# Kernel tuning notes

Hardware: AMD Instinct MI355X
Metric: run time of the kernel (lower is better)

## Reference

```python
import jax, jax.numpy as jnp
import numpy as np

B, T, D_IN, H, NUM_CLASSES = 512, 1024, 4, 64, 1098


def setup_inputs() -> dict:
    key = jax.random.key(0)
    ks = jax.random.split(key, 20)
    s = 1.0 / np.sqrt(H)  # PyTorch LSTM init range

    def w(k, shape):
        return jax.random.uniform(k, shape, jnp.float32, -s, s)

    inp = {}
    inp['x'] = jax.random.normal(ks[0], (B, T, D_IN), jnp.float32)
    lens = jax.random.randint(ks[1], (B,), 1, T + 1)
    inp['lengths'] = jnp.sort(lens)[::-1]  # descending, like pack_sequence
    i = 2
    for layer, d in ((0, D_IN), (1, 2 * H)):
        for dirn in ('f', 'b'):
            inp[f'W_ih_l{layer}{dirn}'] = w(ks[i], (4 * H, d)); i += 1
            inp[f'W_hh_l{layer}{dirn}'] = w(ks[i], (4 * H, H)); i += 1
            inp[f'b_ih_l{layer}{dirn}'] = w(ks[i], (4 * H,)); i += 1
            inp[f'b_hh_l{layer}{dirn}'] = w(ks[i], (4 * H,)); i += 1
    inp['W_out'] = w(ks[i], (NUM_CLASSES, 2 * H)); i += 1
    inp['b_out'] = w(ks[i], (NUM_CLASSES,))
    return inp


def _lstm_layer(x, W_ih, W_hh, b_ih, b_hh):
    # x: [B, T, D] -> outputs [B, T, H]; PyTorch gate order i, f, g, o
    Bb = x.shape[0]
    Hh = W_hh.shape[1]
    xW = jnp.einsum('btd,gd->btg', x, W_ih) + b_ih + b_hh  # [B, T, 4H]

    def step(carry, xt):
        h, c = carry
        g = xt + h @ W_hh.T
        i, f, gg, o = jnp.split(g, 4, axis=-1)
        c = jax.nn.sigmoid(f) * c + jax.nn.sigmoid(i) * jnp.tanh(gg)
        h = jax.nn.sigmoid(o) * jnp.tanh(c)
        return (h, c), h

    init = (jnp.zeros((Bb, Hh), x.dtype), jnp.zeros((Bb, Hh), x.dtype))
    _, hs = jax.lax.scan(step, init, jnp.swapaxes(xW, 0, 1))
    return jnp.swapaxes(hs, 0, 1)


def _reverse_padded(x, lengths):
    # per-sequence time reversal within the valid length (packed-seq semantics)
    Tt = x.shape[1]
    t = jnp.arange(Tt)
    idx = jnp.where(t[None, :] < lengths[:, None], lengths[:, None] - 1 - t[None, :], t[None, :])
    return jnp.take_along_axis(x, idx[:, :, None], axis=1)


def _bidir_layer(x, lengths, pf, pb):
    hf = _lstm_layer(x, *pf)
    hb = _reverse_padded(_lstm_layer(_reverse_padded(x, lengths), *pb), lengths)
    return jnp.concatenate([hf, hb], axis=-1)


def reference(x, lengths,
              W_ih_l0f, W_hh_l0f, b_ih_l0f, b_hh_l0f,
              W_ih_l0b, W_hh_l0b, b_ih_l0b, b_hh_l0b,
              W_ih_l1f, W_hh_l1f, b_ih_l1f, b_hh_l1f,
              W_ih_l1b, W_hh_l1b, b_ih_l1b, b_hh_l1b,
              W_out, b_out):
    h = _bidir_layer(x, lengths,
                     (W_ih_l0f, W_hh_l0f, b_ih_l0f, b_hh_l0f),
                     (W_ih_l0b, W_hh_l0b, b_ih_l0b, b_hh_l0b))
    h = _bidir_layer(h, lengths,
                     (W_ih_l1f, W_hh_l1f, b_ih_l1f, b_hh_l1f),
                     (W_ih_l1b, W_hh_l1b, b_ih_l1b, b_hh_l1b))
    # gather last valid timestep per sequence: [B, 2H]
    lasts = jnp.take_along_axis(h, (lengths - 1)[:, None, None], axis=1)[:, 0]
    return lasts @ W_out.T + b_out
```

## Files before the change

kernel.cpp:

```cpp
#include <hip/hip_runtime.h>
#include <stdint.h>

#define BATCH 512
#define TMAX  1024
#define NC    1098
#define H     64
#define CH    8

typedef __attribute__((ext_vector_type(2))) float    v2;
typedef __attribute__((ext_vector_type(2))) _Float16 h2;

__device__ __forceinline__ v2 mkv2(float a, float b) { v2 r; r.x = a; r.y = b; return r; }
__device__ __forceinline__ float sigmoidf_(float x) { return 1.0f / (1.0f + __expf(-x)); }
__device__ __forceinline__ float tanhf_(float x) { return 1.0f - 2.0f / (__expf(2.0f * x) + 1.0f); }
__device__ __forceinline__ h2 u2h(uint32_t u) { union { uint32_t u; h2 h; } c; c.u = u; return c.h; }

__device__ __forceinline__ float fdot2_(h2 w, h2 x, float acc) {
    return __builtin_amdgcn_fdot2(w, x, acc, false);
}

__global__ __launch_bounds__(256) void lstm_l0(
    const float* __restrict__ x, const int* __restrict__ lengths,
    const float* __restrict__ Wih_f, const float* __restrict__ Whh_f,
    const float* __restrict__ bih_f, const float* __restrict__ bhh_f,
    const float* __restrict__ Wih_b, const float* __restrict__ Whh_b,
    const float* __restrict__ bih_b, const float* __restrict__ bhh_b,
    _Float16* __restrict__ h0 )
{
    const int bk = blockIdx.x;
    const int t = threadIdx.x;
    const int j = t & 63, w = t >> 6;
    const int seq = (w < 2) ? bk : (BATCH - 1 - bk);
    const int dir = w & 1;
    const int xb  = w >> 1;
    const int L = lengths[seq];

    const float* Wih = dir ? Wih_b : Wih_f;
    const float* Whh = dir ? Whh_b : Whh_f;
    const float* bih = dir ? bih_b : bih_f;
    const float* bhh = dir ? bhh_b : bhh_f;

    h2 wh[4][32];
    #pragma unroll
    for (int g = 0; g < 4; g++) {
        const float4* pw = (const float4*)(Whh + (size_t)(64*g + j) * H);
        #pragma unroll
        for (int k = 0; k < 16; k++) {
            float4 a = pw[k];
            h2 lo; lo.x = (_Float16)a.x; lo.y = (_Float16)a.y;
            h2 hi; hi.x = (_Float16)a.z; hi.y = (_Float16)a.w;
            wh[g][2*k]   = lo;
            wh[g][2*k+1] = hi;
        }
    }
    float4 wx[4]; float bb[4];
    #pragma unroll
    for (int g = 0; g < 4; g++) {
        wx[g] = ((const float4*)Wih)[64*g + j];
        bb[g] = bih[64*g + j] + bhh[64*g + j];
    }

    __shared__ __align__(16) float4    xbuf[2][TMAX];
    __shared__ __align__(16) _Float16  hln[4][H];
    {
        const int sA = bk, sB = BATCH - 1 - bk;
        const int LA = lengths[sA], LB = lengths[sB];
        const float4* xA = (const float4*)x + (size_t)sA * TMAX;
        const float4* xB = (const float4*)x + (size_t)sB * TMAX;
        for (int i = t; i < LA; i += 256) xbuf[0][i] = xA[i];
        for (int i = t; i < LB; i += 256) xbuf[1][i] = xB[i];
    }
    hln[w][j] = (_Float16)0.0f;
    float c = 0.0f;
    __syncthreads();

    _Float16* outp = h0 + (size_t)seq * TMAX * 128 + dir * H + j;

    for (int s = 0; s < L; s++) {
        const int tt = dir ? (L - 1 - s) : s;
        const float4 xt = xbuf[xb][tt];
        float p[4];
        #pragma unroll
        for (int g = 0; g < 4; g++)
            p[g] = fmaf(wx[g].w, xt.w, fmaf(wx[g].z, xt.z,
                   fmaf(wx[g].y, xt.y, fmaf(wx[g].x, xt.x, bb[g]))));
        float acA[4] = {0.f,0.f,0.f,0.f}, acB[4] = {0.f,0.f,0.f,0.f};
        const uint4* h4 = (const uint4*)&hln[w][0];
        #pragma unroll
        for (int q = 0; q < 8; q++) {
            uint4 u = h4[q];
            h2 p0 = u2h(u.x), p1 = u2h(u.y), p2 = u2h(u.z), p3 = u2h(u.w);
            #pragma unroll
            for (int g = 0; g < 4; g++) {
                acA[g] = fdot2_(wh[g][4*q+0], p0, acA[g]);
                acA[g] = fdot2_(wh[g][4*q+1], p1, acA[g]);
                acB[g] = fdot2_(wh[g][4*q+2], p2, acB[g]);
                acB[g] = fdot2_(wh[g][4*q+3], p3, acB[g]);
            }
        }
        #pragma unroll
        for (int g = 0; g < 4; g++) p[g] += acA[g] + acB[g];
        const float gi = sigmoidf_(p[0]);
        const float gf = sigmoidf_(p[1]);
        const float gg = tanhf_(p[2]);
        const float go = sigmoidf_(p[3]);
        c = fmaf(gf, c, gi * gg);
        const float h = go * tanhf_(c);
        hln[w][j] = (_Float16)h;
        outp[(size_t)tt * 128] = (_Float16)h;
    }
}

__global__ __launch_bounds__(384) void lstm_l1(
    const _Float16* __restrict__ h0, const int* __restrict__ lengths,
    const float* __restrict__ Wih,  const float* __restrict__ Whh,
    const float* __restrict__ bih,  const float* __restrict__ bhh,
    const float* __restrict__ WihB, const float* __restrict__ bihB,
    const float* __restrict__ bhhB,
    const float* __restrict__ Wout, const float* __restrict__ bout,
    float* __restrict__ out)
{
    const int bk = blockIdx.x;
    const int t = threadIdx.x;
    const int grp = (t >= 192) ? 1 : 0;
    const int tl = t - 192 * grp;
    const int wl = tl >> 6;
    const int l = tl & 63;
    const int seq = grp ? (BATCH - 1 - bk) : bk;
    const int L = lengths[seq];
    const int nch = (L + CH - 1) / CH;
    const int nchMax = (lengths[bk] + CH - 1) / CH;

    __shared__ __align__(16) float    xw[2][2][CH][256];
    __shared__ __align__(16) _Float16 hst[2][2][CH][128];
    __shared__ __align__(16) _Float16 hln[2][H];
    __shared__ __align__(16) float    ybuf[2][2*H];
    __shared__ __align__(16) float    gb[2][192];
    __shared__ __align__(16) float    h0r[2][128];

    const _Float16* hseq = h0 + (size_t)seq * TMAX * 128;

    h2 wsh[128];
    float bb[4] = {0.f, 0.f, 0.f, 0.f};
    int rA = 0, rB = 0;
    if (wl == 0) {
        #pragma unroll
        for (int g = 0; g < 4; g++) {
            const float4* pw = (const float4*)(Whh + (size_t)(64*g + l) * H);
            #pragma unroll
            for (int k = 0; k < 16; k++) {
                float4 a = pw[k];
                h2 lo; lo.x = (_Float16)a.x; lo.y = (_Float16)a.y;
                h2 hi; hi.x = (_Float16)a.z; hi.y = (_Float16)a.w;
                wsh[g*32 + 2*k]   = lo;
                wsh[g*32 + 2*k+1] = hi;
            }
            bb[g] = bih[64*g + l] + bhh[64*g + l];
        }
        hln[grp][l] = (_Float16)0.0f;
    } else {
        const int pw = wl - 1;
        rA = pw * 128 + l; rB = pw * 128 + 64 + l;
        const float4* pa = (const float4*)(Wih + (size_t)rA * 128);
        const float4* pb = (const float4*)(Wih + (size_t)rB * 128);
        #pragma unroll
        for (int k = 0; k < 32; k++) {
            float4 a = pa[k], b2 = pb[k];
            h2 alo; alo.x = (_Float16)a.x;  alo.y = (_Float16)a.y;
            h2 ahi; ahi.x = (_Float16)a.z;  ahi.y = (_Float16)a.w;
            h2 blo; blo.x = (_Float16)b2.x; blo.y = (_Float16)b2.y;
            h2 bhi; bhi.x = (_Float16)b2.z; bhi.y = (_Float16)b2.w;
            wsh[2*k]        = alo;
            wsh[2*k + 1]    = ahi;
            wsh[64 + 2*k]   = blo;
            wsh[64 + 2*k+1] = bhi;
        }
    }

    uint4 st0;
    auto stage_load = [&](int ck) {
        const uint4* gp = (const uint4*)(hseq + (size_t)ck * CH * 128);
        st0 = gp[(wl - 1) * 64 + l];
    };
    auto stage_store = [&](int ck) {
        uint4* dp = (uint4*)&hst[grp][ck & 1][0][0];
        dp[(wl - 1) * 64 + l] = st0;
    };
    auto produce = [&](int ck) {
        const int par = ck & 1;
        for (int r = 0; r < CH; r++) {
            const uint4* rp = (const uint4*)&hst[grp][par][r][0];
            float aA = 0.f, aB = 0.f;
            #pragma unroll
            for (int q = 0; q < 16; q++) {
                uint4 u = rp[q];
                h2 p0 = u2h(u.x), p1 = u2h(u.y), p2 = u2h(u.z), p3 = u2h(u.w);
                aA = fdot2_(wsh[4*q+0], p0, aA);
                aA = fdot2_(wsh[4*q+1], p1, aA);
                aA = fdot2_(wsh[4*q+2], p2, aA);
                aA = fdot2_(wsh[4*q+3], p3, aA);
                aB = fdot2_(wsh[64+4*q+0], p0, aB);
                aB = fdot2_(wsh[64+4*q+1], p1, aB);
                aB = fdot2_(wsh[64+4*q+2], p2, aB);
                aB = fdot2_(wsh[64+4*q+3], p3, aB);
            }
            xw[grp][par][r][rA] = aA;
            xw[grp][par][r][rB] = aB;
        }
    };

    float c = 0.f, h = 0.f;

    if (wl >= 1) { stage_load(0); stage_store(0); if (nch > 1) stage_load(1); }
    __syncthreads();
    if (wl >= 1) { produce(0); if (nch > 1) stage_store(1); }
    __syncthreads();

    for (int cc = 0; cc < nchMax; cc++) {
        if (wl == 0) {
            const int sbeg = cc * CH;
            const int send = (sbeg + CH < L) ? (sbeg + CH) : L;
            const int par = cc & 1;
            for (int s = sbeg; s < send; s++) {
                const int r = s - sbeg;
                float p[4];
                #pragma unroll
                for (int g = 0; g < 4; g++)
                    p[g] = xw[grp][par][r][g*64 + l] + bb[g];
                float acA[4] = {0.f,0.f,0.f,0.f}, acB[4] = {0.f,0.f,0.f,0.f};
                const uint4* h4 = (const uint4*)&hln[grp][0];
                #pragma unroll
                for (int q = 0; q < 8; q++) {
                    uint4 u = h4[q];
                    h2 p0 = u2h(u.x), p1 = u2h(u.y), p2 = u2h(u.z), p3 = u2h(u.w);
                    #pragma unroll
                    for (int g = 0; g < 4; g++) {
                        acA[g] = fdot2_(wsh[g*32+4*q+0], p0, acA[g]);
                        acA[g] = fdot2_(wsh[g*32+4*q+1], p1, acA[g]);
                        acB[g] = fdot2_(wsh[g*32+4*q+2], p2, acB[g]);
                        acB[g] = fdot2_(wsh[g*32+4*q+3], p3, acB[g]);
                    }
                }
                #pragma unroll
                for (int g = 0; g < 4; g++) p[g] += acA[g] + acB[g];
                const float gi = sigmoidf_(p[0]);
                const float gf = sigmoidf_(p[1]);
                const float gg = tanhf_(p[2]);
                const float go = sigmoidf_(p[3]);
                c = fmaf(gf, c, gi * gg);
                h = go * tanhf_(c);
                hln[grp][l] = (_Float16)h;
            }
        } else {
            if (cc + 2 < nch) stage_load(cc + 2);
            if (cc + 1 < nch) produce(cc + 1);
            if (cc + 2 < nch) stage_store(cc + 2);
        }
        __syncthreads();
    }

    if (wl == 0) ybuf[grp][l] = h;
    if (tl < 128) h0r[grp][tl] = (float)hseq[(size_t)(L - 1) * 128 + tl];
    __syncthreads();
    {
        const int row = (tl < 64) ? tl : (tl + 64);
        const float4* wr = (const float4*)(WihB + (size_t)row * 128);
        const float4* xr = (const float4*)&h0r[grp][0];
        v2 a0 = mkv2(bihB[row] + bhhB[row], 0.f), a1 = mkv2(0.f, 0.f);
        #pragma unroll
        for (int k = 0; k < 32; k++) {
            float4 wv = wr[k], xv = xr[k];
            a0 += mkv2(wv.x, wv.y) * mkv2(xv.x, xv.y);
            a1 += mkv2(wv.z, wv.w) * mkv2(xv.z, xv.w);
        }
        const float a = (a0.x + a0.y) + (a1.x + a1.y);
        gb[grp][tl] = (tl >= 64 && tl < 128) ? tanhf_(a) : sigmoidf_(a);
    }
    __syncthreads();
    if (tl < 64) {
        const float hb = gb[grp][128 + tl] * tanhf_(gb[grp][tl] * gb[grp][64 + tl]);
        ybuf[grp][H + tl] = hb;
    }
    __syncthreads();
    const float4* yv = (const float4*)&ybuf[grp][0];
    for (int o = tl; o < NC; o += 192) {
        const float4* wr = (const float4*)(Wout + (size_t)o * 128);
        v2 a0 = mkv2(bout[o], 0.f), a1 = mkv2(0.f, 0.f);
        #pragma unroll
        for (int k = 0; k < 32; k++) {
            float4 wv = wr[k], yy = yv[k];
            a0 += mkv2(wv.x, wv.y) * mkv2(yy.x, yy.y);
            a1 += mkv2(wv.z, wv.w) * mkv2(yy.z, yy.w);
        }
        out[(size_t)seq * NC + o] = (a0.x + a0.y) + (a1.x + a1.y);
    }
}

extern "C" void kernel_launch(void* const* d_in, const int* in_sizes, int n_in,
                              void* d_out, int out_size, void* d_ws, size_t ws_size,
                              hipStream_t stream) {
    const float* x        = (const float*)d_in[0];
    const int*   lengths  = (const int*)  d_in[1];
    const float* Wih_l0f  = (const float*)d_in[2];
    const float* Whh_l0f  = (const float*)d_in[3];
    const float* bih_l0f  = (const float*)d_in[4];
    const float* bhh_l0f  = (const float*)d_in[5];
    const float* Wih_l0b  = (const float*)d_in[6];
    const float* Whh_l0b  = (const float*)d_in[7];
    const float* bih_l0b  = (const float*)d_in[8];
    const float* bhh_l0b  = (const float*)d_in[9];
    const float* Wih_l1f  = (const float*)d_in[10];
    const float* Whh_l1f  = (const float*)d_in[11];
    const float* bih_l1f  = (const float*)d_in[12];
    const float* bhh_l1f  = (const float*)d_in[13];
    const float* Wih_l1b  = (const float*)d_in[14];
    const float* bih_l1b  = (const float*)d_in[16];
    const float* bhh_l1b  = (const float*)d_in[17];
    const float* Wout     = (const float*)d_in[18];
    const float* bout     = (const float*)d_in[19];
    float* out = (float*)d_out;

    _Float16* h0 = (_Float16*)d_ws;

    lstm_l0<<<dim3(BATCH / 2), 256, 0, stream>>>(
        x, lengths,
        Wih_l0f, Whh_l0f, bih_l0f, bhh_l0f,
        Wih_l0b, Whh_l0b, bih_l0b, bhh_l0b, h0);

    lstm_l1<<<dim3(BATCH / 2), 384, 0, stream>>>(
        h0, lengths,
        Wih_l1f, Whh_l1f, bih_l1f, bhh_l1f,
        Wih_l1b, bih_l1b, bhh_l1b, Wout, bout, out);
}
```

Baseline: 1.212 ms.

## Batch 16 sequences per block and use MFMA for layer-0 LSTM recurrence

Layer 0 is restructured so each block handles 16 sequences in one direction, and the recurrent and input projections run as 16x16x32 f16 MFMAs instead of per-thread fdot2 loops. The h state is double-buffered in shared memory with one block barrier per step, and x is prefetched one step ahead from global memory. The grid shrinks from 256 to 64 blocks, so fewer CUs are used. Each block now iterates for the longest length in its group, which wastes steps on shorter sequences.

Result: slower. 1.849 ms (+52.6%).

```diff
diff --git a/kernel.cpp b/kernel.cpp
--- a/kernel.cpp
+++ b/kernel.cpp
@@ -6,9 +6,12 @@
 #define NC    1098
 #define H     64
 #define CH    8
+#define G16   16
 
 typedef __attribute__((ext_vector_type(2))) float    v2;
 typedef __attribute__((ext_vector_type(2))) _Float16 h2;
+typedef __attribute__((ext_vector_type(8))) _Float16 f16x8;
+typedef __attribute__((ext_vector_type(4))) float    f32x4;
 
 __device__ __forceinline__ v2 mkv2(float a, float b) { v2 r; r.x = a; r.y = b; return r; }
 __device__ __forceinline__ float sigmoidf_(float x) { return 1.0f / (1.0f + __expf(-x)); }
@@ -27,87 +30,121 @@
     const float* __restrict__ bih_b, const float* __restrict__ bhh_b,
     _Float16* __restrict__ h0 )
 {
-    const int bk = blockIdx.x;
-    const int t = threadIdx.x;
-    const int j = t & 63, w = t >> 6;
-    const int seq = (w < 2) ? bk : (BATCH - 1 - bk);
-    const int dir = w & 1;
-    const int xb  = w >> 1;
-    const int L = lengths[seq];
+    const int bid = blockIdx.x;
+    const int dir = bid >> 5;
+    const int g   = bid & 31;
+    const int t   = threadIdx.x;
+    const int w   = t >> 6;
+    const int l   = t & 63;
+    const int q   = l >> 4;
+    const int m16 = l & 15;
 
     const float* Wih = dir ? Wih_b : Wih_f;
     const float* Whh = dir ? Whh_b : Whh_f;
     const float* bih = dir ? bih_b : bih_f;
     const float* bhh = dir ? bhh_b : bhh_f;
 
-    h2 wh[4][32];
+    f16x8 bf[4][2];
+    f16x8 bx[4];
+    float bb[4];
     #pragma unroll
-    for (int g = 0; g < 4; g++) {
-        const float4* pw = (const float4*)(Whh + (size_t)(64*g + j) * H);
-        #pragma unroll
-        for (int k = 0; k < 16; k++) {
-            float4 a = pw[k];
-            h2 lo; lo.x = (_Float16)a.x; lo.y = (_Float16)a.y;
-            h2 hi; hi.x = (_Float16)a.z; hi.y = (_Float16)a.w;
-            wh[g][2*k]   = lo;
-            wh[g][2*k+1] = hi;
-        }
-    }
-    float4 wx[4]; float bb[4];
+    for (int tt = 0; tt < 4; tt++) {
+        const int row = tt*64 + 16*w + m16;
+        #pragma unroll
+        for (int kk = 0; kk < 2; kk++) {
+            const float4* p4 = (const float4*)(Whh + (size_t)row * H + kk*32 + 8*q);
+            float4 v0 = p4[0], v1 = p4[1];
+            f16x8 f;
+            f[0]=(_Float16)v0.x; f[1]=(_Float16)v0.y; f[2]=(_Float16)v0.z; f[3]=(_Float16)v0.w;
+            f[4]=(_Float16)v1.x; f[5]=(_Float16)v1.y; f[6]=(_Float16)v1.z; f[7]=(_Float16)v1.w;
+            bf[tt][kk] = f;
+        }
+        f16x8 fx;
+        #pragma unroll
+        for (int j = 0; j < 8; j++) fx[j] = (_Float16)0.0f;
+        if (q == 0) {
+            const float4 xv = *(const float4*)(Wih + (size_t)row * 4);
+            fx[0]=(_Float16)xv.x; fx[1]=(_Float16)xv.y;
+            fx[2]=(_Float16)xv.z; fx[3]=(_Float16)xv.w;
+        }
+        bx[tt] = fx;
+        bb[tt] = bih[row] + bhh[row];
+    }
+
+    const int nsteps = lengths[G16 * g];
+    const int LrA = lengths[G16*g + m16];
+    int Ls[4];
     #pragma unroll
-    for (int g = 0; g < 4; g++) {
-        wx[g] = ((const float4*)Wih)[64*g + j];
-        bb[g] = bih[64*g + j] + bhh[64*g + j];
-    }
-
-    __shared__ __align__(16) float4    xbuf[2][TMAX];
-    __shared__ __align__(16) _Float16  hln[4][H];
-    {
-        const int sA = bk, sB = BATCH - 1 - bk;
-        const int LA = lengths[sA], LB = lengths[sB];
-        const float4* xA = (const float4*)x + (size_t)sA * TMAX;
-        const float4* xB = (const float4*)x + (size_t)sB * TMAX;
-        for (int i = t; i < LA; i += 256) xbuf[0][i] = xA[i];
-        for (int i = t; i < LB; i += 256) xbuf[1][i] = xB[i];
-    }
-    hln[w][j] = (_Float16)0.0f;
-    float c = 0.0f;
-    __syncthreads();
-
-    _Float16* outp = h0 + (size_t)seq * TMAX * 128 + dir * H + j;
-
-    for (int s = 0; s < L; s++) {
-        const int tt = dir ? (L - 1 - s) : s;
-        const float4 xt = xbuf[xb][tt];
-        float p[4];
-        #pragma unroll
-        for (int g = 0; g < 4; g++)
-            p[g] = fmaf(wx[g].w, xt.w, fmaf(wx[g].z, xt.z,
-                   fmaf(wx[g].y, xt.y, fmaf(wx[g].x, xt.x, bb[g]))));
-        float acA[4] = {0.f,0.f,0.f,0.f}, acB[4] = {0.f,0.f,0.f,0.f};
-        const uint4* h4 = (const uint4*)&hln[w][0];
-        #pragma unroll
-        for (int q = 0; q < 8; q++) {
-            uint4 u = h4[q];
-            h2 p0 = u2h(u.x), p1 = u2h(u.y), p2 = u2h(u.z), p3 = u2h(u.w);
-            #pragma unroll
-            for (int g = 0; g < 4; g++) {
-                acA[g] = fdot2_(wh[g][4*q+0], p0, acA[g]);
-                acA[g] = fdot2_(wh[g][4*q+1], p1, acA[g]);
-                acB[g] = fdot2_(wh[g][4*q+2], p2, acB[g]);
-                acB[g] = fdot2_(wh[g][4*q+3], p3, acB[g]);
+    for (int r = 0; r < 4; r++) Ls[r] = lengths[G16*g + 4*q + r];
+
+    __shared__ _Float16 Hb[2][16][72];
+    for (int i = t; i < 2*16*72; i += 256) (&Hb[0][0][0])[i] = (_Float16)0.0f;
+    __syncthreads();
+
+    float c4[4] = {0.f, 0.f, 0.f, 0.f};
+    const float* xrowA = x + (size_t)(G16*g + m16) * TMAX * 4;
+
+    float4 xcur = make_float4(0.f, 0.f, 0.f, 0.f);
+    if (q == 0) {
+        const int tt0 = dir ? (LrA - 1) : 0;
+        xcur = *(const float4*)(xrowA + (size_t)tt0 * 4);
+    }
+
+    int p = 0;
+    for (int s = 0; s < nsteps; s++) {
+        f16x8 a0 = *(const f16x8*)&Hb[p][m16][8*q];
+        f16x8 a1 = *(const f16x8*)&Hb[p][m16][32 + 8*q];
+        f16x8 ax;
+        #pragma unroll
+        for (int j = 0; j < 8; j++) ax[j] = (_Float16)0.0f;
+        if (q == 0) {
+            ax[0]=(_Float16)xcur.x; ax[1]=(_Float16)xcur.y;
+            ax[2]=(_Float16)xcur.z; ax[3]=(_Float16)xcur.w;
+        }
+        float4 xnxt = make_float4(0.f, 0.f, 0.f, 0.f);
+        if (q == 0 && s + 1 < nsteps) {
+            int tn = dir ? (LrA - 2 - s) : (s + 1);
+            tn = tn < 0 ? 0 : (tn >= LrA ? LrA - 1 : tn);
+            xnxt = *(const float4*)(xrowA + (size_t)tn * 4);
+        }
+
+        f32x4 acc0, acc1, acc2, acc3;
+        acc0[0]=bb[0]; acc0[1]=bb[0]; acc0[2]=bb[0]; acc0[3]=bb[0];
+        acc1[0]=bb[1]; acc1[1]=bb[1]; acc1[2]=bb[1]; acc1[3]=bb[1];
+        acc2[0]=bb[2]; acc2[1]=bb[2]; acc2[2]=bb[2]; acc2[3]=bb[2];
+        acc3[0]=bb[3]; acc3[1]=bb[3]; acc3[2]=bb[3]; acc3[3]=bb[3];
+        acc0 = __builtin_amdgcn_mfma_f32_16x16x32_f16(a0, bf[0][0], acc0, 0,0,0);
+        acc1 = __builtin_amdgcn_mfma_f32_16x16x32_f16(a0, bf[1][0], acc1, 0,0,0);
+        acc2 = __builtin_amdgcn_mfma_f32_16x16x32_f16(a0, bf[2][0], acc2, 0,0,0);
+        acc3 = __builtin_amdgcn_mfma_f32_16x16x32_f16(a0, bf[3][0], acc3, 0,0,0);
+        acc0 = __builtin_amdgcn_mfma_f32_16x16x32_f16(a1, bf[0][1], acc0, 0,0,0);
+        acc1 = __builtin_amdgcn_mfma_f32_16x16x32_f16(a1, bf[1][1], acc1, 0,0,0);
+        acc2 = __builtin_amdgcn_mfma_f32_16x16x32_f16(a1, bf[2][1], acc2, 0,0,0);
+        acc3 = __builtin_amdgcn_mfma_f32_16x16x32_f16(a1, bf[3][1], acc3, 0,0,0);
+        acc0 = __builtin_amdgcn_mfma_f32_16x16x32_f16(ax, bx[0], acc0, 0,0,0);
+        acc1 = __builtin_amdgcn_mfma_f32_16x16x32_f16(ax, bx[1], acc1, 0,0,0);
+        acc2 = __builtin_amdgcn_mfma_f32_16x16x32_f16(ax, bx[2], acc2, 0,0,0);
+        acc3 = __builtin_amdgcn_mfma_f32_16x16x32_f16(ax, bx[3], acc3, 0,0,0);
+
+        #pragma unroll
+        for (int r = 0; r < 4; r++) {
+            const float gi = sigmoidf_(acc0[r]);
+            const float gf = sigmoidf_(acc1[r]);
+            const float gg = tanhf_(acc2[r]);
+            const float go = sigmoidf_(acc3[r]);
+            c4[r] = fmaf(gf, c4[r], gi * gg);
+            const float hv = go * tanhf_(c4[r]);
+            const _Float16 hf = (_Float16)hv;
+            Hb[p ^ 1][4*q + r][16*w + m16] = hf;
+            if (s < Ls[r]) {
+                const int seq = G16*g + 4*q + r;
+                const int trt = dir ? (Ls[r] - 1 - s) : s;
+                h0[((size_t)seq * TMAX + trt) * 128 + dir*64 + 16*w + m16] = hf;
             }
         }
-        #pragma unroll
-        for (int g = 0; g < 4; g++) p[g] += acA[g] + acB[g];
-        const float gi = sigmoidf_(p[0]);
-        const float gf = sigmoidf_(p[1]);
-        const float gg = tanhf_(p[2]);
-        const float go = sigmoidf_(p[3]);
-        c = fmaf(gf, c, gi * gg);
-        const float h = go * tanhf_(c);
-        hln[w][j] = (_Float16)h;
-        outp[(size_t)tt * 128] = (_Float16)h;
+        xcur = xnxt;
+        __syncthreads();
+        p ^= 1;
     }
 }
 
@@ -322,7 +359,7 @@
 
     _Float16* h0 = (_Float16*)d_ws;
 
-    lstm_l0<<<dim3(BATCH / 2), 256, 0, stream>>>(
+    lstm_l0<<<dim3(64), 256, 0, stream>>>(
         x, lengths,
         Wih_l0f, Whh_l0f, bih_l0f, bhh_l0f,
         Wih_l0b, Whh_l0b, bih_l0b, bhh_l0b, h0);
```

## Interleave two sequences per wave in layer-0 LSTM to hide recurrence latency

Applied to the files above, without the earlier changes.

Each wave now processes two independent sequences (a long and a short one paired from each end of the length-sorted batch) in one time loop, so the dependent recurrence chains of the two can overlap. The grid for layer 0 shrinks from 256 to 128 blocks. The shared-memory staging of x is dropped in favour of per-step global loads prefetched one step ahead. In exchange there are fewer blocks, which cuts parallelism on a GPU with many CUs, and per-wave work grows.

New measurement: 1.333 ms. +10.0%, slower.

```diff
diff --git a/kernel.cpp b/kernel.cpp
--- a/kernel.cpp
+++ b/kernel.cpp
@@ -30,10 +30,11 @@
     const int bk = blockIdx.x;
     const int t = threadIdx.x;
     const int j = t & 63, w = t >> 6;
-    const int seq = (w < 2) ? bk : (BATCH - 1 - bk);
     const int dir = w & 1;
-    const int xb  = w >> 1;
-    const int L = lengths[seq];
+    const int pr  = w >> 1;
+    const int sA = bk + 128 * pr;
+    const int sB = (pr ? 383 : 511) - bk;
+    const int LA = lengths[sA], LB = lengths[sB];
 
     const float* Wih = dir ? Wih_b : Wih_f;
     const float* Whh = dir ? Whh_b : Whh_f;
@@ -60,54 +61,95 @@
         bb[g] = bih[64*g + j] + bhh[64*g + j];
     }
 
-    __shared__ __align__(16) float4    xbuf[2][TMAX];
-    __shared__ __align__(16) _Float16  hln[4][H];
-    {
-        const int sA = bk, sB = BATCH - 1 - bk;
-        const int LA = lengths[sA], LB = lengths[sB];
-        const float4* xA = (const float4*)x + (size_t)sA * TMAX;
-        const float4* xB = (const float4*)x + (size_t)sB * TMAX;
-        for (int i = t; i < LA; i += 256) xbuf[0][i] = xA[i];
-        for (int i = t; i < LB; i += 256) xbuf[1][i] = xB[i];
-    }
-    hln[w][j] = (_Float16)0.0f;
-    float c = 0.0f;
-    __syncthreads();
-
-    _Float16* outp = h0 + (size_t)seq * TMAX * 128 + dir * H + j;
-
-    for (int s = 0; s < L; s++) {
-        const int tt = dir ? (L - 1 - s) : s;
-        const float4 xt = xbuf[xb][tt];
-        float p[4];
+    __shared__ __align__(16) _Float16 hln[8][H];
+    hln[2*w + 0][j] = (_Float16)0.0f;
+    hln[2*w + 1][j] = (_Float16)0.0f;
+
+    float cA = 0.0f, cB = 0.0f;
+    const float* xrA = x + (size_t)sA * TMAX * 4;
+    const float* xrB = x + (size_t)sB * TMAX * 4;
+    float4 xA = *(const float4*)(xrA + (size_t)(dir ? (LA - 1) : 0) * 4);
+    float4 xB = *(const float4*)(xrB + (size_t)(dir ? (LB - 1) : 0) * 4);
+
+    _Float16* opA = h0 + (size_t)sA * TMAX * 128 + dir * H + j;
+    _Float16* opB = h0 + (size_t)sB * TMAX * 128 + dir * H + j;
+
+    for (int s = 0; s < LA; s++) {
+        const bool doB = (s < LB);
+        const int ttA = dir ? (LA - 1 - s) : s;
+        const int ttB = dir ? (LB - 1 - s) : s;
+        float4 xnA = make_float4(0.f,0.f,0.f,0.f);
+        float4 xnB = make_float4(0.f,0.f,0.f,0.f);
+        if (s + 1 < LA) xnA = *(const float4*)(xrA + (size_t)(dir ? (LA-2-s) : (s+1)) * 4);
+        if (s + 1 < LB) xnB = *(const float4*)(xrB + (size_t)(dir ? (LB-2-s) : (s+1)) * 4);
+
+        float pA[4];
         #pragma unroll
         for (int g = 0; g < 4; g++)
-            p[g] = fmaf(wx[g].w, xt.w, fmaf(wx[g].z, xt.z,
-                   fmaf(wx[g].y, xt.y, fmaf(wx[g].x, xt.x, bb[g]))));
-        float acA[4] = {0.f,0.f,0.f,0.f}, acB[4] = {0.f,0.f,0.f,0.f};
-        const uint4* h4 = (const uint4*)&hln[w][0];
-        #pragma unroll
-        for (int q = 0; q < 8; q++) {
-            uint4 u = h4[q];
-            h2 p0 = u2h(u.x), p1 = u2h(u.y), p2 = u2h(u.z), p3 = u2h(u.w);
-            #pragma unroll
-            for (int g = 0; g < 4; g++) {
-                acA[g] = fdot2_(wh[g][4*q+0], p0, acA[g]);
-                acA[g] = fdot2_(wh[g][4*q+1], p1, acA[g]);
-                acB[g] = fdot2_(wh[g][4*q+2], p2, acB[g]);
-                acB[g] = fdot2_(wh[g][4*q+3], p3, acB[g]);
-            }
-        }
-        #pragma unroll
-        for (int g = 0; g < 4; g++) p[g] += acA[g] + acB[g];
-        const float gi = sigmoidf_(p[0]);
-        const float gf = sigmoidf_(p[1]);
-        const float gg = tanhf_(p[2]);
-        const float go = sigmoidf_(p[3]);
-        c = fmaf(gf, c, gi * gg);
-        const float h = go * tanhf_(c);
-        hln[w][j] = (_Float16)h;
-        outp[(size_t)tt * 128] = (_Float16)h;
+            pA[g] = fmaf(wx[g].w, xA.w, fmaf(wx[g].z, xA.z,
+                    fmaf(wx[g].y, xA.y, fmaf(wx[g].x, xA.x, bb[g]))));
+        float aA[4] = {0.f,0.f,0.f,0.f}, bA[4] = {0.f,0.f,0.f,0.f};
+        {
+            const uint4* h4 = (const uint4*)&hln[2*w + 0][0];
+            #pragma unroll
+            for (int q = 0; q < 8; q++) {
+                uint4 u = h4[q];
+                h2 p0 = u2h(u.x), p1 = u2h(u.y), p2 = u2h(u.z), p3 = u2h(u.w);
+                #pragma unroll
+                for (int g = 0; g < 4; g++) {
+                    aA[g] = fdot2_(wh[g][4*q+0], p0, aA[g]);
+                    aA[g] = fdot2_(wh[g][4*q+1], p1, aA[g]);
+                    bA[g] = fdot2_(wh[g][4*q+2], p2, bA[g]);
+                    bA[g] = fdot2_(wh[g][4*q+3], p3, bA[g]);
+                }
+            }
+        }
+        #pragma unroll
+        for (int g = 0; g < 4; g++) pA[g] += aA[g] + bA[g];
+        {
+            const float gi = sigmoidf_(pA[0]);
+            const float gf = sigmoidf_(pA[1]);
+            const float gg = tanhf_(pA[2]);
+            const float go = sigmoidf_(pA[3]);
+            cA = fmaf(gf, cA, gi * gg);
+            const float hv = go * tanhf_(cA);
+            hln[2*w + 0][j] = (_Float16)hv;
+            opA[(size_t)ttA * 128] = (_Float16)hv;
+        }
+
+        if (doB) {
+            float pB[4];
+            #pragma unroll
+            for (int g = 0; g < 4; g++)
+                pB[g] = fmaf(wx[g].w, xB.w, fmaf(wx[g].z, xB.z,
+                        fmaf(wx[g].y, xB.y, fmaf(wx[g].x, xB.x, bb[g]))));
+            float aB[4] = {0.f,0.f,0.f,0.f}, bB[4] = {0.f,0.f,0.f,0.f};
+            const uint4* h4 = (const uint4*)&hln[2*w + 1][0];
+            #pragma unroll
+            for (int q = 0; q < 8; q++) {
+                uint4 u = h4[q];
+                h2 p0 = u2h(u.x), p1 = u2h(u.y), p2 = u2h(u.z), p3 = u2h(u.w);
+                #pragma unroll
+                for (int g = 0; g < 4; g++) {
+                    aB[g] = fdot2_(wh[g][4*q+0], p0, aB[g]);
+                    aB[g] = fdot2_(wh[g][4*q+1], p1, aB[g]);
+                    bB[g] = fdot2_(wh[g][4*q+2], p2, bB[g]);
+                    bB[g] = fdot2_(wh[g][4*q+3], p3, bB[g]);
+                }
+            }
+            #pragma unroll
+            for (int g = 0; g < 4; g++) pB[g] += aB[g] + bB[g];
+            const float gi = sigmoidf_(pB[0]);
+            const float gf = sigmoidf_(pB[1]);
+            const float gg = tanhf_(pB[2]);
+            const float go = sigmoidf_(pB[3]);
+            cB = fmaf(gf, cB, gi * gg);
+            const float hv = go * tanhf_(cB);
+            hln[2*w + 1][j] = (_Float16)hv;
+            opB[(size_t)ttB * 128] = (_Float16)hv;
+        }
+        xA = xnA;
+        if (doB) xB = xnB;
     }
 }
 
@@ -322,7 +364,7 @@
 
     _Float16* h0 = (_Float16*)d_ws;
 
-    lstm_l0<<<dim3(BATCH / 2), 256, 0, stream>>>(
+    lstm_l0<<<dim3(128), 256, 0, stream>>>(
         x, lengths,
         Wih_l0f, Whh_l0f, bih_l0f, bhh_l0f,
         Wih_l0b, Whh_l0b, bih_l0b, bhh_l0b, h0);
```

## Split layer-0 LSTM into one block per sequence and double the layer-1 chunk size

Applied to the files above, without the earlier changes.

Layer 0 now launches one 128-thread block per sequence, covering forward and backward directions, instead of pairing a long and a short sequence in a 256-thread block. This lets the scheduler balance uneven sequence lengths. Layer 1 doubles the chunk length, so each producer stages two rows per step and the block synchronises half as often. The consumer wave is also moved to a different wave position in the first group. Larger chunks need more shared memory and registers, which may lower occupancy.

After: 1.208 ms. Within noise of the previous version (-0.3%).

```diff
diff --git a/kernel.cpp b/kernel.cpp
--- a/kernel.cpp
+++ b/kernel.cpp
@@ -5,7 +5,7 @@
 #define TMAX  1024
 #define NC    1098
 #define H     64
-#define CH    8
+#define CH    16
 
 typedef __attribute__((ext_vector_type(2))) float    v2;
 typedef __attribute__((ext_vector_type(2))) _Float16 h2;
@@ -19,7 +19,7 @@
     return __builtin_amdgcn_fdot2(w, x, acc, false);
 }
 
-__global__ __launch_bounds__(256) void lstm_l0(
+__global__ __launch_bounds__(128) void lstm_l0(
     const float* __restrict__ x, const int* __restrict__ lengths,
     const float* __restrict__ Wih_f, const float* __restrict__ Whh_f,
     const float* __restrict__ bih_f, const float* __restrict__ bhh_f,
@@ -27,13 +27,10 @@
     const float* __restrict__ bih_b, const float* __restrict__ bhh_b,
     _Float16* __restrict__ h0 )
 {
-    const int bk = blockIdx.x;
+    const int b = blockIdx.x;
     const int t = threadIdx.x;
-    const int j = t & 63, w = t >> 6;
-    const int seq = (w < 2) ? bk : (BATCH - 1 - bk);
-    const int dir = w & 1;
-    const int xb  = w >> 1;
-    const int L = lengths[seq];
+    const int j = t & 63, dir = t >> 6;
+    const int L = lengths[b];
 
     const float* Wih = dir ? Wih_b : Wih_f;
     const float* Whh = dir ? Whh_b : Whh_f;
@@ -60,32 +57,28 @@
         bb[g] = bih[64*g + j] + bhh[64*g + j];
     }
 
-    __shared__ __align__(16) float4    xbuf[2][TMAX];
-    __shared__ __align__(16) _Float16  hln[4][H];
+    __shared__ __align__(16) float4    xbuf[TMAX];
+    __shared__ __align__(16) _Float16  hb16[2][H];
     {
-        const int sA = bk, sB = BATCH - 1 - bk;
-        const int LA = lengths[sA], LB = lengths[sB];
-        const float4* xA = (const float4*)x + (size_t)sA * TMAX;
-        const float4* xB = (const float4*)x + (size_t)sB * TMAX;
-        for (int i = t; i < LA; i += 256) xbuf[0][i] = xA[i];
-        for (int i = t; i < LB; i += 256) xbuf[1][i] = xB[i];
-    }
-    hln[w][j] = (_Float16)0.0f;
+        const float4* x4 = (const float4*)x + (size_t)b * TMAX;
+        for (int i = t; i < L; i += 128) xbuf[i] = x4[i];
+    }
+    hb16[dir][j] = (_Float16)0.0f;
     float c = 0.0f;
     __syncthreads();
 
-    _Float16* outp = h0 + (size_t)seq * TMAX * 128 + dir * H + j;
+    _Float16* outp = h0 + (size_t)b * TMAX * 128 + dir * H + j;
 
     for (int s = 0; s < L; s++) {
         const int tt = dir ? (L - 1 - s) : s;
-        const float4 xt = xbuf[xb][tt];
+        const float4 xt = xbuf[tt];
         float p[4];
         #pragma unroll
         for (int g = 0; g < 4; g++)
             p[g] = fmaf(wx[g].w, xt.w, fmaf(wx[g].z, xt.z,
                    fmaf(wx[g].y, xt.y, fmaf(wx[g].x, xt.x, bb[g]))));
         float acA[4] = {0.f,0.f,0.f,0.f}, acB[4] = {0.f,0.f,0.f,0.f};
-        const uint4* h4 = (const uint4*)&hln[w][0];
+        const uint4* h4 = (const uint4*)&hb16[dir][0];
         #pragma unroll
         for (int q = 0; q < 8; q++) {
             uint4 u = h4[q];
@@ -106,7 +99,7 @@
         const float go = sigmoidf_(p[3]);
         c = fmaf(gf, c, gi * gg);
         const float h = go * tanhf_(c);
-        hln[w][j] = (_Float16)h;
+        hb16[dir][j] = (_Float16)h;
         outp[(size_t)tt * 128] = (_Float16)h;
     }
 }
@@ -124,8 +117,10 @@
     const int t = threadIdx.x;
     const int grp = (t >= 192) ? 1 : 0;
     const int tl = t - 192 * grp;
-    const int wl = tl >> 6;
+    const int tlw = tl >> 6;
     const int l = tl & 63;
+    const bool isCons = grp ? (tlw == 0) : (tlw == 2);
+    const int prodIdx = grp ? (tlw - 1) : tlw;
     const int seq = grp ? (BATCH - 1 - bk) : bk;
     const int L = lengths[seq];
     const int nch = (L + CH - 1) / CH;
@@ -143,7 +138,7 @@
     h2 wsh[128];
     float bb[4] = {0.f, 0.f, 0.f, 0.f};
     int rA = 0, rB = 0;
-    if (wl == 0) {
+    if (isCons) {
         #pragma unroll
         for (int g = 0; g < 4; g++) {
             const float4* pw = (const float4*)(Whh + (size_t)(64*g + l) * H);
@@ -159,8 +154,7 @@
         }
         hln[grp][l] = (_Float16)0.0f;
     } else {
-        const int pw = wl - 1;
-        rA = pw * 128 + l; rB = pw * 128 + 64 + l;
+        rA = prodIdx * 128 + l; rB = prodIdx * 128 + 64 + l;
         const float4* pa = (const float4*)(Wih + (size_t)rA * 128);
         const float4* pb = (const float4*)(Wih + (size_t)rB * 128);
         #pragma unroll
@@ -177,14 +171,16 @@
         }
     }
 
-    uint4 st0;
+    uint4 st0, st1;
     auto stage_load = [&](int ck) {
         const uint4* gp = (const uint4*)(hseq + (size_t)ck * CH * 128);
-        st0 = gp[(wl - 1) * 64 + l];
+        st0 = gp[prodIdx * 64 + l];
+        st1 = gp[128 + prodIdx * 64 + l];
     };
     auto stage_store = [&](int ck) {
         uint4* dp = (uint4*)&hst[grp][ck & 1][0][0];
-        dp[(wl - 1) * 64 + l] = st0;
+        dp[prodIdx * 64 + l] = st0;
+        dp[128 + prodIdx * 64 + l] = st1;
     };
     auto produce = [&](int ck) {
         const int par = ck & 1;
@@ -211,13 +207,13 @@
 
     float c = 0.f, h = 0.f;
 
-    if (wl >= 1) { stage_load(0); stage_store(0); if (nch > 1) stage_load(1); }
-    __syncthreads();
-    if (wl >= 1) { produce(0); if (nch > 1) stage_store(1); }
+    if (!isCons) { stage_load(0); stage_store(0); if (nch > 1) stage_load(1); }
+    __syncthreads();
+    if (!isCons) { produce(0); if (nch > 1) stage_store(1); }
     __syncthreads();
 
     for (int cc = 0; cc < nchMax; cc++) {
-        if (wl == 0) {
+        if (isCons) {
             const int sbeg = cc * CH;
             const int send = (sbeg + CH < L) ? (sbeg + CH) : L;
             const int par = cc & 1;
@@ -259,7 +255,7 @@
         __syncthreads();
     }
 
-    if (wl == 0) ybuf[grp][l] = h;
+    if (isCons) ybuf[grp][l] = h;
     if (tl < 128) h0r[grp][tl] = (float)hseq[(size_t)(L - 1) * 128 + tl];
     __syncthreads();
     {
@@ -322,7 +318,7 @@
 
     _Float16* h0 = (_Float16*)d_ws;
 
-    lstm_l0<<<dim3(BATCH / 2), 256, 0, stream>>>(
+    lstm_l0<<<dim3(BATCH), 128, 0, stream>>>(
         x, lengths,
         Wih_l0f, Whh_l0f, bih_l0f, bhh_l0f,
         Wih_l0b, Whh_l0b, bih_l0b, bhh_l0b, h0);
```
